# Kernel optimization log

Hardware: AMD Instinct MI355X
Metric: run time of the kernel (lower is better)

## Reference

```python
import jax, jax.numpy as jnp
import numpy as np

N_NODES = 50000
N_EDGES = 640000
IN_CH, HID_CH, OUT_CH = 128, 128, 64


def setup_inputs() -> dict:
    key = jax.random.key(0)
    ks = jax.random.split(key, 12)
    def glorot(k, fan_in, fan_out):
        s = jnp.sqrt(6.0 / (fan_in + fan_out))
        return jax.random.uniform(k, (fan_in, fan_out), jnp.float32, -s, s)
    x = jax.random.normal(ks[0], (N_NODES, IN_CH), jnp.float32)
    edge_index = jax.random.randint(ks[1], (2, N_EDGES), 0, N_NODES, jnp.int64)
    return {
        "x": x,
        "edge_index": edge_index,
        "W1": glorot(ks[2], IN_CH, HID_CH), "b1": jnp.zeros((HID_CH,), jnp.float32),
        "W2": glorot(ks[3], HID_CH, HID_CH), "b2": jnp.zeros((HID_CH,), jnp.float32),
        "W3": glorot(ks[4], HID_CH, OUT_CH), "b3": jnp.zeros((OUT_CH,), jnp.float32),
        "Wres": glorot(ks[5], IN_CH, OUT_CH), "bres": jnp.zeros((OUT_CH,), jnp.float32),
    }


def _gcn_norm(edge_index, n):
    # add self-loops, then symmetric normalization deg^-1/2[row]*deg^-1/2[col]
    sl = jnp.arange(n, dtype=edge_index.dtype)
    row = jnp.concatenate([edge_index[0], sl])
    col = jnp.concatenate([edge_index[1], sl])
    deg = jnp.zeros((n,), jnp.float32).at[col].add(1.0)
    dinv = jnp.where(deg > 0, jax.lax.rsqrt(deg), 0.0)
    norm = dinv[row] * dinv[col]  # [E+N]
    return row, col, norm


def _gcn_conv(x, W, b, row, col, norm, n):
    h = x @ W                          # linear transform first (PyG GCNConv)
    msg = h[row] * norm[:, None]       # gather + scale: [E+N, d]
    out = jax.ops.segment_sum(msg, col, num_segments=n)  # scatter-add
    return out + b


def reference(x, edge_index, W1, b1, W2, b2, W3, b3, Wres, bres):
    n = x.shape[0]
    row, col, norm = _gcn_norm(edge_index, n)
    # dropout is inference-mode identity (training=False)
    h = jax.nn.relu(_gcn_conv(x, W1, b1, row, col, norm, n))
    h = jax.nn.relu(_gcn_conv(h, W2, b2, row, col, norm, n))
    h = _gcn_conv(h, W3, b3, row, col, norm, n)
    residual = x @ Wres + bres
    return h + residual
```

## Files before the change

kernel.cpp:

```cpp
#include <hip/hip_runtime.h>

#define N_NODES 50000
#define N_EDGES 640000


__global__ void k_init(int* __restrict__ cnt, int* __restrict__ cursor) {
    int i = blockIdx.x * blockDim.x + threadIdx.x;
    if (i < N_NODES) { cnt[i] = 0; cursor[i] = 0; }
}

__global__ void k_count(const int* __restrict__ ei, int* __restrict__ cnt) {
    int e = blockIdx.x * blockDim.x + threadIdx.x;
    if (e < N_EDGES) atomicAdd(&cnt[ei[N_EDGES + e]], 1);
}

__global__ void k_dinv(const int* __restrict__ cnt, float* __restrict__ dinv) {
    int i = blockIdx.x * blockDim.x + threadIdx.x;
    if (i < N_NODES) dinv[i] = rsqrtf((float)(cnt[i] + 1));
}


__global__ void k_scan1(const int* __restrict__ cnt, int* __restrict__ offsets,
                        int* __restrict__ partials) {
    __shared__ int s[256];
    int t = threadIdx.x;
    int i = blockIdx.x * 256 + t;
    int v = (i < N_NODES) ? cnt[i] : 0;
    s[t] = v;
    __syncthreads();
    #pragma unroll
    for (int d = 1; d < 256; d <<= 1) {
        int add = (t >= d) ? s[t - d] : 0;
        __syncthreads();
        s[t] += add;
        __syncthreads();
    }
    if (i < N_NODES) offsets[i + 1] = s[t];
    if (t == 255) partials[blockIdx.x] = s[255];
    if (i == 0) offsets[0] = 0;
}

__global__ void k_scan2(int* __restrict__ partials, int nb) {
    __shared__ int s[256];
    int t = threadIdx.x;
    int v = (t < nb) ? partials[t] : 0;
    s[t] = v;
    __syncthreads();
    #pragma unroll
    for (int d = 1; d < 256; d <<= 1) {
        int add = (t >= d) ? s[t - d] : 0;
        __syncthreads();
        s[t] += add;
        __syncthreads();
    }
    if (t < nb) partials[t] = s[t] - v;
}

__global__ void k_scan3(int* __restrict__ offsets, const int* __restrict__ partials) {
    int i = blockIdx.x * 256 + threadIdx.x;
    if (i < N_NODES) offsets[i + 1] += partials[blockIdx.x];
}


__global__ void k_fill(const int* __restrict__ ei, const float* __restrict__ dinv,
                       const int* __restrict__ offsets, int* __restrict__ cursor,
                       int* __restrict__ csr_src, float* __restrict__ csr_w) {
    int e = blockIdx.x * blockDim.x + threadIdx.x;
    if (e < N_EDGES) {
        int r = ei[e];
        int c = ei[N_EDGES + e];
        float w = dinv[r] * dinv[c];
        int p = atomicAdd(&cursor[c], 1);
        int idx = offsets[c] + p;
        csr_src[idx] = r;
        csr_w[idx] = w;
    }
}


template <int OUTC>
__global__ __launch_bounds__(256, (OUTC == 128 ? 2 : 3))
void k_gemm(const float* __restrict__ A, const float* __restrict__ W,
            const float* __restrict__ bias, float* __restrict__ C) {
    constexpr int CG = OUTC / 4;
    constexpr int TR = CG / 8;
    __shared__ float sW[128 * OUTC];
    __shared__ float sX[32 * 128];

    int t = threadIdx.x;
    int row0 = blockIdx.x * 32;

    for (int i = t; i < 128 * OUTC / 4; i += 256)
        ((float4*)sW)[i] = ((const float4*)W)[i];
    for (int i = t; i < 1024; i += 256) {
        int r = i >> 5, c4 = i & 31;
        int gr = row0 + r;
        float4 v = make_float4(0.f, 0.f, 0.f, 0.f);
        if (gr < N_NODES) v = ((const float4*)(A + (size_t)gr * 128))[c4];
        ((float4*)sX)[i] = v;
    }
    __syncthreads();

    int tx = t % CG;
    int ty = t / CG;
    float acc[TR][4];
    #pragma unroll
    for (int rr = 0; rr < TR; ++rr) { acc[rr][0]=0.f; acc[rr][1]=0.f; acc[rr][2]=0.f; acc[rr][3]=0.f; }

    #pragma unroll 8
    for (int k = 0; k < 128; ++k) {
        float4 wv = ((const float4*)sW)[k * CG + tx];
        #pragma unroll
        for (int rr = 0; rr < TR; ++rr) {
            float xv = sX[(ty * TR + rr) * 128 + k];
            acc[rr][0] = fmaf(xv, wv.x, acc[rr][0]);
            acc[rr][1] = fmaf(xv, wv.y, acc[rr][1]);
            acc[rr][2] = fmaf(xv, wv.z, acc[rr][2]);
            acc[rr][3] = fmaf(xv, wv.w, acc[rr][3]);
        }
    }

    float4 bv = make_float4(0.f, 0.f, 0.f, 0.f);
    if (bias) bv = ((const float4*)bias)[tx];
    #pragma unroll
    for (int rr = 0; rr < TR; ++rr) {
        int gr = row0 + ty * TR + rr;
        if (gr < N_NODES) {
            float4 o = make_float4(acc[rr][0] + bv.x, acc[rr][1] + bv.y,
                                   acc[rr][2] + bv.z, acc[rr][3] + bv.w);
            ((float4*)(C + (size_t)gr * OUTC))[tx] = o;
        }
    }
}


template <int CH, bool RELU, bool HASADD>
__global__ __launch_bounds__(256)
void k_agg(const float* __restrict__ T, const int* __restrict__ offs,
           const int* __restrict__ csr_src, const float* __restrict__ csr_w,
           const float* __restrict__ dinv, const float* __restrict__ bias,
           const float* __restrict__ add, float* __restrict__ O) {
    int lane = threadIdx.x & 63;
    int v = blockIdx.x * 4 + (threadIdx.x >> 6);
    if (v >= N_NODES) return;
    int beg = offs[v], end = offs[v + 1];
    float di = dinv[v];
    float sw = di * di;

    if constexpr (CH == 128) {
        float2 hself = ((const float2*)(T + (size_t)v * 128))[lane];
        float a0 = sw * hself.x, a1 = sw * hself.y;
        int j = beg;
        for (; j + 4 <= end; j += 4) {
            int   s0 = csr_src[j],   s1 = csr_src[j+1], s2 = csr_src[j+2], s3 = csr_src[j+3];
            float w0 = csr_w[j],     w1 = csr_w[j+1],   w2 = csr_w[j+2],   w3 = csr_w[j+3];
            float2 h0 = ((const float2*)(T + (size_t)s0 * 128))[lane];
            float2 h1 = ((const float2*)(T + (size_t)s1 * 128))[lane];
            float2 h2 = ((const float2*)(T + (size_t)s2 * 128))[lane];
            float2 h3 = ((const float2*)(T + (size_t)s3 * 128))[lane];
            a0 = fmaf(w0, h0.x, fmaf(w1, h1.x, fmaf(w2, h2.x, fmaf(w3, h3.x, a0))));
            a1 = fmaf(w0, h0.y, fmaf(w1, h1.y, fmaf(w2, h2.y, fmaf(w3, h3.y, a1))));
        }
        for (; j < end; ++j) {
            int s = csr_src[j]; float w = csr_w[j];
            float2 hh = ((const float2*)(T + (size_t)s * 128))[lane];
            a0 = fmaf(w, hh.x, a0);
            a1 = fmaf(w, hh.y, a1);
        }
        a0 += bias[2 * lane];
        a1 += bias[2 * lane + 1];
        if constexpr (HASADD) {
            a0 += add[(size_t)v * 128 + 2 * lane];
            a1 += add[(size_t)v * 128 + 2 * lane + 1];
        }
        if constexpr (RELU) { a0 = fmaxf(a0, 0.f); a1 = fmaxf(a1, 0.f); }
        ((float2*)(O + (size_t)v * 128))[lane] = make_float2(a0, a1);
    } else {
        float a = sw * T[(size_t)v * 64 + lane];
        int j = beg;
        for (; j + 4 <= end; j += 4) {
            int   s0 = csr_src[j],   s1 = csr_src[j+1], s2 = csr_src[j+2], s3 = csr_src[j+3];
            float w0 = csr_w[j],     w1 = csr_w[j+1],   w2 = csr_w[j+2],   w3 = csr_w[j+3];
            float h0 = T[(size_t)s0 * 64 + lane];
            float h1 = T[(size_t)s1 * 64 + lane];
            float h2 = T[(size_t)s2 * 64 + lane];
            float h3 = T[(size_t)s3 * 64 + lane];
            a = fmaf(w0, h0, fmaf(w1, h1, fmaf(w2, h2, fmaf(w3, h3, a))));
        }
        for (; j < end; ++j) {
            int s = csr_src[j]; float w = csr_w[j];
            a = fmaf(w, T[(size_t)s * 64 + lane], a);
        }
        a += bias[lane];
        if constexpr (HASADD) a += add[(size_t)v * 64 + lane];
        if constexpr (RELU) a = fmaxf(a, 0.f);
        O[(size_t)v * 64 + lane] = a;
    }
}


extern "C" void kernel_launch(void* const* d_in, const int* in_sizes, int n_in,
                              void* d_out, int out_size, void* d_ws, size_t ws_size,
                              hipStream_t stream) {
    const float* x    = (const float*)d_in[0];
    const int*   ei   = (const int*)d_in[1];
    const float* W1   = (const float*)d_in[2];
    const float* b1   = (const float*)d_in[3];
    const float* W2   = (const float*)d_in[4];
    const float* b2   = (const float*)d_in[5];
    const float* W3   = (const float*)d_in[6];
    const float* b3   = (const float*)d_in[7];
    const float* Wres = (const float*)d_in[8];
    const float* bres = (const float*)d_in[9];
    float* out = (float*)d_out;

    char* base = (char*)d_ws;
    int*   cnt      = (int*)(base);
    int*   cursor   = (int*)(base + 200704);
    float* dinv     = (float*)(base + 2 * 200704);
    int*   offsets  = (int*)(base + 3 * 200704);
    int*   partials = (int*)(base + 4 * 200704);
    int*   csr_src  = (int*)(base + 4 * 200704 + 1024);
    float* csr_w    = (float*)(base + 4 * 200704 + 1024 + 2560000);
    float* bufA     = (float*)(base + 4 * 200704 + 1024 + 2 * 2560000);
    float* bufB     = bufA + (size_t)N_NODES * 128;

    const int NB_N = (N_NODES + 255) / 256;
    const int NB_E = (N_EDGES + 255) / 256;
    const int NB_G = (N_NODES + 31) / 32;
    const int NB_A = (N_NODES + 3) / 4;

    k_init <<<NB_N, 256, 0, stream>>>(cnt, cursor);
    k_count<<<NB_E, 256, 0, stream>>>(ei, cnt);
    k_dinv <<<NB_N, 256, 0, stream>>>(cnt, dinv);
    k_scan1<<<NB_N, 256, 0, stream>>>(cnt, offsets, partials);
    k_scan2<<<1,    256, 0, stream>>>(partials, NB_N);
    k_scan3<<<NB_N, 256, 0, stream>>>(offsets, partials);
    k_fill <<<NB_E, 256, 0, stream>>>(ei, dinv, offsets, cursor, csr_src, csr_w);

    k_gemm<128><<<NB_G, 256, 0, stream>>>(x, W1, nullptr, bufA);
    k_agg<128, true, false><<<NB_A, 256, 0, stream>>>(bufA, offsets, csr_src, csr_w, dinv, b1, nullptr, bufB);
    k_gemm<128><<<NB_G, 256, 0, stream>>>(bufB, W2, nullptr, bufA);
    k_agg<128, true, false><<<NB_A, 256, 0, stream>>>(bufA, offsets, csr_src, csr_w, dinv, b2, nullptr, bufB);
    k_gemm<64><<<NB_G, 256, 0, stream>>>(bufB, W3, nullptr, bufA);
    k_gemm<64><<<NB_G, 256, 0, stream>>>(x, Wres, bres, bufB);
    k_agg<64, false, true><<<NB_A, 256, 0, stream>>>(bufA, offsets, csr_src, csr_w, dinv, b3, bufB, out);
}
```

Before: 416.8 us.

## Fuse GCN aggregation with following GEMM and residual via shared-memory tiles

Each aggregation kernel now gathers 128 nodes into shared memory and immediately multiplies them by the next layer's weight matrix, so the intermediate aggregated activations never go to global memory. The final layer also computes the residual x@Wres+bres in the same kernel, and the dinv computation is folded into the scan. This removes several launches and global round trips. In exchange, weights are read straight from global/L1 instead of LDS, the 64KB LDS tile and 512-thread blocks limit occupancy, and each wave handles 16 nodes serially, which reduces the latency hiding available for the gather.

```diff
diff --git a/kernel.cpp b/kernel.cpp
--- a/kernel.cpp
+++ b/kernel.cpp
@@ -14,18 +14,13 @@
     if (e < N_EDGES) atomicAdd(&cnt[ei[N_EDGES + e]], 1);
 }
 
-__global__ void k_dinv(const int* __restrict__ cnt, float* __restrict__ dinv) {
-    int i = blockIdx.x * blockDim.x + threadIdx.x;
-    if (i < N_NODES) dinv[i] = rsqrtf((float)(cnt[i] + 1));
-}
-
-
 __global__ void k_scan1(const int* __restrict__ cnt, int* __restrict__ offsets,
-                        int* __restrict__ partials) {
+                        int* __restrict__ partials, float* __restrict__ dinv) {
     __shared__ int s[256];
     int t = threadIdx.x;
     int i = blockIdx.x * 256 + t;
     int v = (i < N_NODES) ? cnt[i] : 0;
+    if (i < N_NODES) dinv[i] = rsqrtf((float)(v + 1));
     s[t] = v;
     __syncthreads();
     #pragma unroll
@@ -60,7 +55,6 @@
     int i = blockIdx.x * 256 + threadIdx.x;
     if (i < N_NODES) offsets[i + 1] += partials[blockIdx.x];
 }
-
 
 __global__ void k_fill(const int* __restrict__ ei, const float* __restrict__ dinv,
                        const int* __restrict__ offsets, int* __restrict__ cursor,
@@ -78,123 +72,209 @@
 }
 
 
+__global__ __launch_bounds__(512, 4)
+void k_gemm_x(const float* __restrict__ A, const float* __restrict__ W,
+              float* __restrict__ O) {
+    int t = threadIdx.x;
+    int tx = t & 31;
+    int ty = t >> 5;
+    int base = blockIdx.x * 128;
+
+    float acc[8][4];
+    #pragma unroll
+    for (int r = 0; r < 8; ++r) { acc[r][0]=0.f; acc[r][1]=0.f; acc[r][2]=0.f; acc[r][3]=0.f; }
+
+    int rows[8];
+    #pragma unroll
+    for (int r = 0; r < 8; ++r) {
+        int gr = base + ty * 8 + r;
+        rows[r] = (gr < N_NODES) ? gr : (N_NODES - 1);
+    }
+
+    #pragma unroll 2
+    for (int k = 0; k < 128; k += 4) {
+        float4 w0 = ((const float4*)(W + (size_t)(k + 0) * 128))[tx];
+        float4 w1 = ((const float4*)(W + (size_t)(k + 1) * 128))[tx];
+        float4 w2 = ((const float4*)(W + (size_t)(k + 2) * 128))[tx];
+        float4 w3 = ((const float4*)(W + (size_t)(k + 3) * 128))[tx];
+        #pragma unroll
+        for (int r = 0; r < 8; ++r) {
+            float4 xv = *(const float4*)(A + (size_t)rows[r] * 128 + k);
+            acc[r][0] = fmaf(xv.x, w0.x, fmaf(xv.y, w1.x, fmaf(xv.z, w2.x, fmaf(xv.w, w3.x, acc[r][0]))));
+            acc[r][1] = fmaf(xv.x, w0.y, fmaf(xv.y, w1.y, fmaf(xv.z, w2.y, fmaf(xv.w, w3.y, acc[r][1]))));
+            acc[r][2] = fmaf(xv.x, w0.z, fmaf(xv.y, w1.z, fmaf(xv.z, w2.z, fmaf(xv.w, w3.z, acc[r][2]))));
+            acc[r][3] = fmaf(xv.x, w0.w, fmaf(xv.y, w1.w, fmaf(xv.z, w2.w, fmaf(xv.w, w3.w, acc[r][3]))));
+        }
+    }
+
+    #pragma unroll
+    for (int r = 0; r < 8; ++r) {
+        int gr = base + ty * 8 + r;
+        if (gr < N_NODES)
+            ((float4*)(O + (size_t)gr * 128))[tx] =
+                make_float4(acc[r][0], acc[r][1], acc[r][2], acc[r][3]);
+    }
+}
+
+
 template <int OUTC>
-__global__ __launch_bounds__(256, (OUTC == 128 ? 2 : 3))
-void k_gemm(const float* __restrict__ A, const float* __restrict__ W,
-            const float* __restrict__ bias, float* __restrict__ C) {
+__global__ __launch_bounds__(512, 4)
+void k_agg_gemm(const float* __restrict__ T, const int* __restrict__ offs,
+                const int* __restrict__ csr_src, const float* __restrict__ csr_w,
+                const float* __restrict__ dinv, const float* __restrict__ ba,
+                const float* __restrict__ W, float* __restrict__ O) {
+    __shared__ float sh[128 * 128];
+    int t = threadIdx.x;
+    int wave = t >> 6, lane = t & 63;
+    int base = blockIdx.x * 128;
+
+    for (int i = 0; i < 16; ++i) {
+        int vl = wave * 16 + i;
+        int v = base + vl;
+        float a0 = 0.f, a1 = 0.f;
+        if (v < N_NODES) {
+            float di = dinv[v];
+            float sw = di * di;
+            float2 hs = ((const float2*)(T + (size_t)v * 128))[lane];
+            a0 = sw * hs.x; a1 = sw * hs.y;
+            int beg = offs[v], end = offs[v + 1];
+            int j = beg;
+            for (; j + 4 <= end; j += 4) {
+                int   s0 = csr_src[j],   s1 = csr_src[j+1], s2 = csr_src[j+2], s3 = csr_src[j+3];
+                float w0 = csr_w[j],     w1 = csr_w[j+1],   w2 = csr_w[j+2],   w3 = csr_w[j+3];
+                float2 h0 = ((const float2*)(T + (size_t)s0 * 128))[lane];
+                float2 h1 = ((const float2*)(T + (size_t)s1 * 128))[lane];
+                float2 h2 = ((const float2*)(T + (size_t)s2 * 128))[lane];
+                float2 h3 = ((const float2*)(T + (size_t)s3 * 128))[lane];
+                a0 = fmaf(w0, h0.x, fmaf(w1, h1.x, fmaf(w2, h2.x, fmaf(w3, h3.x, a0))));
+                a1 = fmaf(w0, h0.y, fmaf(w1, h1.y, fmaf(w2, h2.y, fmaf(w3, h3.y, a1))));
+            }
+            for (; j < end; ++j) {
+                int s = csr_src[j]; float w = csr_w[j];
+                float2 hh = ((const float2*)(T + (size_t)s * 128))[lane];
+                a0 = fmaf(w, hh.x, a0);
+                a1 = fmaf(w, hh.y, a1);
+            }
+            a0 = fmaxf(a0 + ba[2 * lane], 0.f);
+            a1 = fmaxf(a1 + ba[2 * lane + 1], 0.f);
+        }
+        ((float2*)(sh + vl * 128))[lane] = make_float2(a0, a1);
+    }
+    __syncthreads();
+
     constexpr int CG = OUTC / 4;
-    constexpr int TR = CG / 8;
-    __shared__ float sW[128 * OUTC];
-    __shared__ float sX[32 * 128];
-
-    int t = threadIdx.x;
-    int row0 = blockIdx.x * 32;
-
-    for (int i = t; i < 128 * OUTC / 4; i += 256)
-        ((float4*)sW)[i] = ((const float4*)W)[i];
-    for (int i = t; i < 1024; i += 256) {
-        int r = i >> 5, c4 = i & 31;
-        int gr = row0 + r;
-        float4 v = make_float4(0.f, 0.f, 0.f, 0.f);
-        if (gr < N_NODES) v = ((const float4*)(A + (size_t)gr * 128))[c4];
-        ((float4*)sX)[i] = v;
-    }
-    __syncthreads();
-
+    constexpr int TR = CG / 4;
     int tx = t % CG;
     int ty = t / CG;
+
     float acc[TR][4];
     #pragma unroll
-    for (int rr = 0; rr < TR; ++rr) { acc[rr][0]=0.f; acc[rr][1]=0.f; acc[rr][2]=0.f; acc[rr][3]=0.f; }
-
-    #pragma unroll 8
-    for (int k = 0; k < 128; ++k) {
-        float4 wv = ((const float4*)sW)[k * CG + tx];
+    for (int r = 0; r < TR; ++r) { acc[r][0]=0.f; acc[r][1]=0.f; acc[r][2]=0.f; acc[r][3]=0.f; }
+
+    #pragma unroll 2
+    for (int k = 0; k < 128; k += 4) {
+        float4 w0 = ((const float4*)(W + (size_t)(k + 0) * OUTC))[tx];
+        float4 w1 = ((const float4*)(W + (size_t)(k + 1) * OUTC))[tx];
+        float4 w2 = ((const float4*)(W + (size_t)(k + 2) * OUTC))[tx];
+        float4 w3 = ((const float4*)(W + (size_t)(k + 3) * OUTC))[tx];
         #pragma unroll
-        for (int rr = 0; rr < TR; ++rr) {
-            float xv = sX[(ty * TR + rr) * 128 + k];
-            acc[rr][0] = fmaf(xv, wv.x, acc[rr][0]);
-            acc[rr][1] = fmaf(xv, wv.y, acc[rr][1]);
-            acc[rr][2] = fmaf(xv, wv.z, acc[rr][2]);
-            acc[rr][3] = fmaf(xv, wv.w, acc[rr][3]);
-        }
-    }
-
-    float4 bv = make_float4(0.f, 0.f, 0.f, 0.f);
-    if (bias) bv = ((const float4*)bias)[tx];
-    #pragma unroll
-    for (int rr = 0; rr < TR; ++rr) {
-        int gr = row0 + ty * TR + rr;
+        for (int r = 0; r < TR; ++r) {
+            float4 xv = *(const float4*)(sh + (ty * TR + r) * 128 + k);
+            acc[r][0] = fmaf(xv.x, w0.x, fmaf(xv.y, w1.x, fmaf(xv.z, w2.x, fmaf(xv.w, w3.x, acc[r][0]))));
+            acc[r][1] = fmaf(xv.x, w0.y, fmaf(xv.y, w1.y, fmaf(xv.z, w2.y, fmaf(xv.w, w3.y, acc[r][1]))));
+            acc[r][2] = fmaf(xv.x, w0.z, fmaf(xv.y, w1.z, fmaf(xv.z, w2.z, fmaf(xv.w, w3.z, acc[r][2]))));
+            acc[r][3] = fmaf(xv.x, w0.w, fmaf(xv.y, w1.w, fmaf(xv.z, w2.w, fmaf(xv.w, w3.w, acc[r][3]))));
+        }
+    }
+
+    #pragma unroll
+    for (int r = 0; r < TR; ++r) {
+        int gr = base + ty * TR + r;
+        if (gr < N_NODES)
+            ((float4*)(O + (size_t)gr * OUTC))[tx] =
+                make_float4(acc[r][0], acc[r][1], acc[r][2], acc[r][3]);
+    }
+}
+
+
+__global__ __launch_bounds__(512, 4)
+void k_agg64_res(const float* __restrict__ T, const int* __restrict__ offs,
+                 const int* __restrict__ csr_src, const float* __restrict__ csr_w,
+                 const float* __restrict__ dinv, const float* __restrict__ b3,
+                 const float* __restrict__ x, const float* __restrict__ Wres,
+                 const float* __restrict__ bres, float* __restrict__ out) {
+    __shared__ float sh[128 * 64];
+    int t = threadIdx.x;
+    int wave = t >> 6, lane = t & 63;
+    int base = blockIdx.x * 128;
+
+    for (int i = 0; i < 16; ++i) {
+        int vl = wave * 16 + i;
+        int v = base + vl;
+        float a = 0.f;
+        if (v < N_NODES) {
+            float di = dinv[v];
+            float sw = di * di;
+            a = sw * T[(size_t)v * 64 + lane];
+            int beg = offs[v], end = offs[v + 1];
+            int j = beg;
+            for (; j + 4 <= end; j += 4) {
+                int   s0 = csr_src[j],   s1 = csr_src[j+1], s2 = csr_src[j+2], s3 = csr_src[j+3];
+                float w0 = csr_w[j],     w1 = csr_w[j+1],   w2 = csr_w[j+2],   w3 = csr_w[j+3];
+                float h0 = T[(size_t)s0 * 64 + lane];
+                float h1 = T[(size_t)s1 * 64 + lane];
+                float h2 = T[(size_t)s2 * 64 + lane];
+                float h3 = T[(size_t)s3 * 64 + lane];
+                a = fmaf(w0, h0, fmaf(w1, h1, fmaf(w2, h2, fmaf(w3, h3, a))));
+            }
+            for (; j < end; ++j)
+                a = fmaf(csr_w[j], T[(size_t)csr_src[j] * 64 + lane], a);
+            a += b3[lane];
+        }
+        sh[vl * 64 + lane] = a;
+    }
+    __syncthreads();
+
+    int tx = t & 15;
+    int ty = t >> 4;
+    float acc[4][4];
+    #pragma unroll
+    for (int r = 0; r < 4; ++r) { acc[r][0]=0.f; acc[r][1]=0.f; acc[r][2]=0.f; acc[r][3]=0.f; }
+
+    int rows[4];
+    #pragma unroll
+    for (int r = 0; r < 4; ++r) {
+        int gr = base + ty * 4 + r;
+        rows[r] = (gr < N_NODES) ? gr : (N_NODES - 1);
+    }
+
+    #pragma unroll 2
+    for (int k = 0; k < 128; k += 4) {
+        float4 w0 = ((const float4*)(Wres + (size_t)(k + 0) * 64))[tx];
+        float4 w1 = ((const float4*)(Wres + (size_t)(k + 1) * 64))[tx];
+        float4 w2 = ((const float4*)(Wres + (size_t)(k + 2) * 64))[tx];
+        float4 w3 = ((const float4*)(Wres + (size_t)(k + 3) * 64))[tx];
+        #pragma unroll
+        for (int r = 0; r < 4; ++r) {
+            float4 xv = *(const float4*)(x + (size_t)rows[r] * 128 + k);
+            acc[r][0] = fmaf(xv.x, w0.x, fmaf(xv.y, w1.x, fmaf(xv.z, w2.x, fmaf(xv.w, w3.x, acc[r][0]))));
+            acc[r][1] = fmaf(xv.x, w0.y, fmaf(xv.y, w1.y, fmaf(xv.z, w2.y, fmaf(xv.w, w3.y, acc[r][1]))));
+            acc[r][2] = fmaf(xv.x, w0.z, fmaf(xv.y, w1.z, fmaf(xv.z, w2.z, fmaf(xv.w, w3.z, acc[r][2]))));
+            acc[r][3] = fmaf(xv.x, w0.w, fmaf(xv.y, w1.w, fmaf(xv.z, w2.w, fmaf(xv.w, w3.w, acc[r][3]))));
+        }
+    }
+
+    float4 bv = ((const float4*)bres)[tx];
+    #pragma unroll
+    for (int r = 0; r < 4; ++r) {
+        int vl = ty * 4 + r;
+        int gr = base + vl;
         if (gr < N_NODES) {
-            float4 o = make_float4(acc[rr][0] + bv.x, acc[rr][1] + bv.y,
-                                   acc[rr][2] + bv.z, acc[rr][3] + bv.w);
-            ((float4*)(C + (size_t)gr * OUTC))[tx] = o;
-        }
-    }
-}
-
-
-template <int CH, bool RELU, bool HASADD>
-__global__ __launch_bounds__(256)
-void k_agg(const float* __restrict__ T, const int* __restrict__ offs,
-           const int* __restrict__ csr_src, const float* __restrict__ csr_w,
-           const float* __restrict__ dinv, const float* __restrict__ bias,
-           const float* __restrict__ add, float* __restrict__ O) {
-    int lane = threadIdx.x & 63;
-    int v = blockIdx.x * 4 + (threadIdx.x >> 6);
-    if (v >= N_NODES) return;
-    int beg = offs[v], end = offs[v + 1];
-    float di = dinv[v];
-    float sw = di * di;
-
-    if constexpr (CH == 128) {
-        float2 hself = ((const float2*)(T + (size_t)v * 128))[lane];
-        float a0 = sw * hself.x, a1 = sw * hself.y;
-        int j = beg;
-        for (; j + 4 <= end; j += 4) {
-            int   s0 = csr_src[j],   s1 = csr_src[j+1], s2 = csr_src[j+2], s3 = csr_src[j+3];
-            float w0 = csr_w[j],     w1 = csr_w[j+1],   w2 = csr_w[j+2],   w3 = csr_w[j+3];
-            float2 h0 = ((const float2*)(T + (size_t)s0 * 128))[lane];
-            float2 h1 = ((const float2*)(T + (size_t)s1 * 128))[lane];
-            float2 h2 = ((const float2*)(T + (size_t)s2 * 128))[lane];
-            float2 h3 = ((const float2*)(T + (size_t)s3 * 128))[lane];
-            a0 = fmaf(w0, h0.x, fmaf(w1, h1.x, fmaf(w2, h2.x, fmaf(w3, h3.x, a0))));
-            a1 = fmaf(w0, h0.y, fmaf(w1, h1.y, fmaf(w2, h2.y, fmaf(w3, h3.y, a1))));
-        }
-        for (; j < end; ++j) {
-            int s = csr_src[j]; float w = csr_w[j];
-            float2 hh = ((const float2*)(T + (size_t)s * 128))[lane];
-            a0 = fmaf(w, hh.x, a0);
-            a1 = fmaf(w, hh.y, a1);
-        }
-        a0 += bias[2 * lane];
-        a1 += bias[2 * lane + 1];
-        if constexpr (HASADD) {
-            a0 += add[(size_t)v * 128 + 2 * lane];
-            a1 += add[(size_t)v * 128 + 2 * lane + 1];
-        }
-        if constexpr (RELU) { a0 = fmaxf(a0, 0.f); a1 = fmaxf(a1, 0.f); }
-        ((float2*)(O + (size_t)v * 128))[lane] = make_float2(a0, a1);
-    } else {
-        float a = sw * T[(size_t)v * 64 + lane];
-        int j = beg;
-        for (; j + 4 <= end; j += 4) {
-            int   s0 = csr_src[j],   s1 = csr_src[j+1], s2 = csr_src[j+2], s3 = csr_src[j+3];
-            float w0 = csr_w[j],     w1 = csr_w[j+1],   w2 = csr_w[j+2],   w3 = csr_w[j+3];
-            float h0 = T[(size_t)s0 * 64 + lane];
-            float h1 = T[(size_t)s1 * 64 + lane];
-            float h2 = T[(size_t)s2 * 64 + lane];
-            float h3 = T[(size_t)s3 * 64 + lane];
-            a = fmaf(w0, h0, fmaf(w1, h1, fmaf(w2, h2, fmaf(w3, h3, a))));
-        }
-        for (; j < end; ++j) {
-            int s = csr_src[j]; float w = csr_w[j];
-            a = fmaf(w, T[(size_t)s * 64 + lane], a);
-        }
-        a += bias[lane];
-        if constexpr (HASADD) a += add[(size_t)v * 64 + lane];
-        if constexpr (RELU) a = fmaxf(a, 0.f);
-        O[(size_t)v * 64 + lane] = a;
+            float4 s = ((const float4*)(sh + vl * 64))[tx];
+            ((float4*)(out + (size_t)gr * 64))[tx] =
+                make_float4(acc[r][0] + bv.x + s.x, acc[r][1] + bv.y + s.y,
+                            acc[r][2] + bv.z + s.z, acc[r][3] + bv.w + s.w);
+        }
     }
 }
 
@@ -227,22 +307,17 @@
 
     const int NB_N = (N_NODES + 255) / 256;
     const int NB_E = (N_EDGES + 255) / 256;
-    const int NB_G = (N_NODES + 31) / 32;
-    const int NB_A = (N_NODES + 3) / 4;
+    const int NB_F = (N_NODES + 127) / 128;
 
     k_init <<<NB_N, 256, 0, stream>>>(cnt, cursor);
     k_count<<<NB_E, 256, 0, stream>>>(ei, cnt);
-    k_dinv <<<NB_N, 256, 0, stream>>>(cnt, dinv);
-    k_scan1<<<NB_N, 256, 0, stream>>>(cnt, offsets, partials);
+    k_scan1<<<NB_N, 256, 0, stream>>>(cnt, offsets, partials, dinv);
     k_scan2<<<1,    256, 0, stream>>>(partials, NB_N);
     k_scan3<<<NB_N, 256, 0, stream>>>(offsets, partials);
     k_fill <<<NB_E, 256, 0, stream>>>(ei, dinv, offsets, cursor, csr_src, csr_w);
 
-    k_gemm<128><<<NB_G, 256, 0, stream>>>(x, W1, nullptr, bufA);
-    k_agg<128, true, false><<<NB_A, 256, 0, stream>>>(bufA, offsets, csr_src, csr_w, dinv, b1, nullptr, bufB);
-    k_gemm<128><<<NB_G, 256, 0, stream>>>(bufB, W2, nullptr, bufA);
-    k_agg<128, true, false><<<NB_A, 256, 0, stream>>>(bufA, offsets, csr_src, csr_w, dinv, b2, nullptr, bufB);
-    k_gemm<64><<<NB_G, 256, 0, stream>>>(bufB, W3, nullptr, bufA);
-    k_gemm<64><<<NB_G, 256, 0, stream>>>(x, Wres, bres, bufB);
-    k_agg<64, false, true><<<NB_A, 256, 0, stream>>>(bufA, offsets, csr_src, csr_w, dinv, b3, bufB, out);
-}
+    k_gemm_x<<<NB_F, 512, 0, stream>>>(x, W1, bufA);
+    k_agg_gemm<128><<<NB_F, 512, 0, stream>>>(bufA, offsets, csr_src, csr_w, dinv, b1, W2, bufB);
+    k_agg_gemm<64><<<NB_F, 512, 0, stream>>>(bufB, offsets, csr_src, csr_w, dinv, b2, W3, bufA);
+    k_agg64_res<<<NB_F, 512, 0, stream>>>(bufA, offsets, csr_src, csr_w, dinv, b3, x, Wres, bres, out);
+}
```

Measured after the change: 494.9 us. 1.19x slower.

## Store transformed features in fp16 for gathers and drop shared-memory GEMM tiling

Applied to the files above, without the earlier changes.

The GEMM outputs that feed each aggregation are now written as fp16, so the irregular neighbour gathers move half the bytes. The GEMM drops its shared-memory staging of W and X. Each thread instead reads W and A directly from global memory/cache over an 8-row register tile, and the occupancy hint is raised. The degree-inverse computation is folded into the first scan kernel to remove one launch. The fp16 intermediates lose precision relative to the fp32 reference, and the GEMM now relies on cache hits instead of LDS reuse.

```diff
diff --git a/kernel.cpp b/kernel.cpp
--- a/kernel.cpp
+++ b/kernel.cpp
@@ -1,4 +1,5 @@
 #include <hip/hip_runtime.h>
+#include <hip/hip_fp16.h>
 
 #define N_NODES 50000
 #define N_EDGES 640000
@@ -14,18 +15,13 @@
     if (e < N_EDGES) atomicAdd(&cnt[ei[N_EDGES + e]], 1);
 }
 
-__global__ void k_dinv(const int* __restrict__ cnt, float* __restrict__ dinv) {
-    int i = blockIdx.x * blockDim.x + threadIdx.x;
-    if (i < N_NODES) dinv[i] = rsqrtf((float)(cnt[i] + 1));
-}
-
-
 __global__ void k_scan1(const int* __restrict__ cnt, int* __restrict__ offsets,
-                        int* __restrict__ partials) {
+                        int* __restrict__ partials, float* __restrict__ dinv) {
     __shared__ int s[256];
     int t = threadIdx.x;
     int i = blockIdx.x * 256 + t;
     int v = (i < N_NODES) ? cnt[i] : 0;
+    if (i < N_NODES) dinv[i] = rsqrtf((float)(v + 1));
     s[t] = v;
     __syncthreads();
     #pragma unroll
@@ -60,7 +56,6 @@
     int i = blockIdx.x * 256 + threadIdx.x;
     if (i < N_NODES) offsets[i + 1] += partials[blockIdx.x];
 }
-
 
 __global__ void k_fill(const int* __restrict__ ei, const float* __restrict__ dinv,
                        const int* __restrict__ offsets, int* __restrict__ cursor,
@@ -78,65 +73,75 @@
 }
 
 
-template <int OUTC>
-__global__ __launch_bounds__(256, (OUTC == 128 ? 2 : 3))
+template <int OUTC, bool HALF_OUT>
+__global__ __launch_bounds__(256, 4)
 void k_gemm(const float* __restrict__ A, const float* __restrict__ W,
-            const float* __restrict__ bias, float* __restrict__ C) {
+            const float* __restrict__ bias, void* __restrict__ O) {
     constexpr int CG = OUTC / 4;
-    constexpr int TR = CG / 8;
-    __shared__ float sW[128 * OUTC];
-    __shared__ float sX[32 * 128];
+    constexpr int RG = 256 / CG;
+    constexpr int TR = 8;
+    constexpr int BM = RG * TR;
 
     int t = threadIdx.x;
-    int row0 = blockIdx.x * 32;
-
-    for (int i = t; i < 128 * OUTC / 4; i += 256)
-        ((float4*)sW)[i] = ((const float4*)W)[i];
-    for (int i = t; i < 1024; i += 256) {
-        int r = i >> 5, c4 = i & 31;
-        int gr = row0 + r;
-        float4 v = make_float4(0.f, 0.f, 0.f, 0.f);
-        if (gr < N_NODES) v = ((const float4*)(A + (size_t)gr * 128))[c4];
-        ((float4*)sX)[i] = v;
-    }
-    __syncthreads();
-
     int tx = t % CG;
     int ty = t / CG;
+    int base = blockIdx.x * BM;
+
     float acc[TR][4];
     #pragma unroll
-    for (int rr = 0; rr < TR; ++rr) { acc[rr][0]=0.f; acc[rr][1]=0.f; acc[rr][2]=0.f; acc[rr][3]=0.f; }
-
-    #pragma unroll 8
-    for (int k = 0; k < 128; ++k) {
-        float4 wv = ((const float4*)sW)[k * CG + tx];
+    for (int r = 0; r < TR; ++r) { acc[r][0]=0.f; acc[r][1]=0.f; acc[r][2]=0.f; acc[r][3]=0.f; }
+
+    int rows[TR];
+    #pragma unroll
+    for (int r = 0; r < TR; ++r) {
+        int gr = base + ty * TR + r;
+        rows[r] = (gr < N_NODES) ? gr : (N_NODES - 1);
+    }
+
+    #pragma unroll 2
+    for (int k = 0; k < 128; k += 4) {
+        float4 w0 = ((const float4*)(W + (size_t)(k + 0) * OUTC))[tx];
+        float4 w1 = ((const float4*)(W + (size_t)(k + 1) * OUTC))[tx];
+        float4 w2 = ((const float4*)(W + (size_t)(k + 2) * OUTC))[tx];
+        float4 w3 = ((const float4*)(W + (size_t)(k + 3) * OUTC))[tx];
         #pragma unroll
-        for (int rr = 0; rr < TR; ++rr) {
-            float xv = sX[(ty * TR + rr) * 128 + k];
-            acc[rr][0] = fmaf(xv, wv.x, acc[rr][0]);
-            acc[rr][1] = fmaf(xv, wv.y, acc[rr][1]);
-            acc[rr][2] = fmaf(xv, wv.z, acc[rr][2]);
-            acc[rr][3] = fmaf(xv, wv.w, acc[rr][3]);
+        for (int r = 0; r < TR; ++r) {
+            float4 xv = *(const float4*)(A + (size_t)rows[r] * 128 + k);
+            acc[r][0] = fmaf(xv.x, w0.x, fmaf(xv.y, w1.x, fmaf(xv.z, w2.x, fmaf(xv.w, w3.x, acc[r][0]))));
+            acc[r][1] = fmaf(xv.x, w0.y, fmaf(xv.y, w1.y, fmaf(xv.z, w2.y, fmaf(xv.w, w3.y, acc[r][1]))));
+            acc[r][2] = fmaf(xv.x, w0.z, fmaf(xv.y, w1.z, fmaf(xv.z, w2.z, fmaf(xv.w, w3.z, acc[r][2]))));
+            acc[r][3] = fmaf(xv.x, w0.w, fmaf(xv.y, w1.w, fmaf(xv.z, w2.w, fmaf(xv.w, w3.w, acc[r][3]))));
         }
     }
 
     float4 bv = make_float4(0.f, 0.f, 0.f, 0.f);
     if (bias) bv = ((const float4*)bias)[tx];
     #pragma unroll
-    for (int rr = 0; rr < TR; ++rr) {
-        int gr = row0 + ty * TR + rr;
+    for (int r = 0; r < TR; ++r) {
+        int gr = base + ty * TR + r;
         if (gr < N_NODES) {
-            float4 o = make_float4(acc[rr][0] + bv.x, acc[rr][1] + bv.y,
-                                   acc[rr][2] + bv.z, acc[rr][3] + bv.w);
-            ((float4*)(C + (size_t)gr * OUTC))[tx] = o;
-        }
-    }
-}
-
-
-template <int CH, bool RELU, bool HASADD>
+            if constexpr (HALF_OUT) {
+                __half* Oh = (__half*)O;
+                ushort4 p = make_ushort4(
+                    __half_as_ushort(__float2half_rn(acc[r][0] + bv.x)),
+                    __half_as_ushort(__float2half_rn(acc[r][1] + bv.y)),
+                    __half_as_ushort(__float2half_rn(acc[r][2] + bv.z)),
+                    __half_as_ushort(__float2half_rn(acc[r][3] + bv.w)));
+                *(ushort4*)(Oh + (size_t)gr * OUTC + tx * 4) = p;
+            } else {
+                float* Of = (float*)O;
+                ((float4*)(Of + (size_t)gr * OUTC))[tx] =
+                    make_float4(acc[r][0] + bv.x, acc[r][1] + bv.y,
+                                acc[r][2] + bv.z, acc[r][3] + bv.w);
+            }
+        }
+    }
+}
+
+
+template <int CH, bool RELU, bool HASADD, bool HALF_IN>
 __global__ __launch_bounds__(256)
-void k_agg(const float* __restrict__ T, const int* __restrict__ offs,
+void k_agg(const void* __restrict__ Tv, const int* __restrict__ offs,
            const int* __restrict__ csr_src, const float* __restrict__ csr_w,
            const float* __restrict__ dinv, const float* __restrict__ bias,
            const float* __restrict__ add, float* __restrict__ O) {
@@ -148,22 +153,28 @@
     float sw = di * di;
 
     if constexpr (CH == 128) {
-        float2 hself = ((const float2*)(T + (size_t)v * 128))[lane];
-        float a0 = sw * hself.x, a1 = sw * hself.y;
+        auto LD = [&](int s) -> float2 {
+            if constexpr (HALF_IN)
+                return __half22float2(((const __half2*)((const __half*)Tv + (size_t)s * 128))[lane]);
+            else
+                return ((const float2*)((const float*)Tv + (size_t)s * 128))[lane];
+        };
+        float2 hs = LD(v);
+        float a0 = sw * hs.x, a1 = sw * hs.y;
         int j = beg;
         for (; j + 4 <= end; j += 4) {
             int   s0 = csr_src[j],   s1 = csr_src[j+1], s2 = csr_src[j+2], s3 = csr_src[j+3];
             float w0 = csr_w[j],     w1 = csr_w[j+1],   w2 = csr_w[j+2],   w3 = csr_w[j+3];
-            float2 h0 = ((const float2*)(T + (size_t)s0 * 128))[lane];
-            float2 h1 = ((const float2*)(T + (size_t)s1 * 128))[lane];
-            float2 h2 = ((const float2*)(T + (size_t)s2 * 128))[lane];
-            float2 h3 = ((const float2*)(T + (size_t)s3 * 128))[lane];
+            float2 h0 = LD(s0);
+            float2 h1 = LD(s1);
+            float2 h2 = LD(s2);
+            float2 h3 = LD(s3);
             a0 = fmaf(w0, h0.x, fmaf(w1, h1.x, fmaf(w2, h2.x, fmaf(w3, h3.x, a0))));
             a1 = fmaf(w0, h0.y, fmaf(w1, h1.y, fmaf(w2, h2.y, fmaf(w3, h3.y, a1))));
         }
         for (; j < end; ++j) {
-            int s = csr_src[j]; float w = csr_w[j];
-            float2 hh = ((const float2*)(T + (size_t)s * 128))[lane];
+            float w = csr_w[j];
+            float2 hh = LD(csr_src[j]);
             a0 = fmaf(w, hh.x, a0);
             a1 = fmaf(w, hh.y, a1);
         }
@@ -176,21 +187,25 @@
         if constexpr (RELU) { a0 = fmaxf(a0, 0.f); a1 = fmaxf(a1, 0.f); }
         ((float2*)(O + (size_t)v * 128))[lane] = make_float2(a0, a1);
     } else {
-        float a = sw * T[(size_t)v * 64 + lane];
+        auto LD1 = [&](int s) -> float {
+            if constexpr (HALF_IN)
+                return __half2float(((const __half*)Tv)[(size_t)s * 64 + lane]);
+            else
+                return ((const float*)Tv)[(size_t)s * 64 + lane];
+        };
+        float a = sw * LD1(v);
         int j = beg;
         for (; j + 4 <= end; j += 4) {
             int   s0 = csr_src[j],   s1 = csr_src[j+1], s2 = csr_src[j+2], s3 = csr_src[j+3];
             float w0 = csr_w[j],     w1 = csr_w[j+1],   w2 = csr_w[j+2],   w3 = csr_w[j+3];
-            float h0 = T[(size_t)s0 * 64 + lane];
-            float h1 = T[(size_t)s1 * 64 + lane];
-            float h2 = T[(size_t)s2 * 64 + lane];
-            float h3 = T[(size_t)s3 * 64 + lane];
+            float h0 = LD1(s0);
+            float h1 = LD1(s1);
+            float h2 = LD1(s2);
+            float h3 = LD1(s3);
             a = fmaf(w0, h0, fmaf(w1, h1, fmaf(w2, h2, fmaf(w3, h3, a))));
         }
-        for (; j < end; ++j) {
-            int s = csr_src[j]; float w = csr_w[j];
-            a = fmaf(w, T[(size_t)s * 64 + lane], a);
-        }
+        for (; j < end; ++j)
+            a = fmaf(csr_w[j], LD1(csr_src[j]), a);
         a += bias[lane];
         if constexpr (HASADD) a += add[(size_t)v * 64 + lane];
         if constexpr (RELU) a = fmaxf(a, 0.f);
@@ -215,34 +230,35 @@
     float* out = (float*)d_out;
 
     char* base = (char*)d_ws;
-    int*   cnt      = (int*)(base);
-    int*   cursor   = (int*)(base + 200704);
-    float* dinv     = (float*)(base + 2 * 200704);
-    int*   offsets  = (int*)(base + 3 * 200704);
-    int*   partials = (int*)(base + 4 * 200704);
-    int*   csr_src  = (int*)(base + 4 * 200704 + 1024);
-    float* csr_w    = (float*)(base + 4 * 200704 + 1024 + 2560000);
-    float* bufA     = (float*)(base + 4 * 200704 + 1024 + 2 * 2560000);
-    float* bufB     = bufA + (size_t)N_NODES * 128;
+    int*    cnt      = (int*)(base);
+    int*    cursor   = (int*)(base + 200704);
+    float*  dinv     = (float*)(base + 2 * 200704);
+    int*    offsets  = (int*)(base + 3 * 200704);
+    int*    partials = (int*)(base + 4 * 200704);
+    int*    csr_src  = (int*)(base + 4 * 200704 + 1024);
+    float*  csr_w    = (float*)(base + 4 * 200704 + 1024 + 2560000);
+    float*  bufA     = (float*)(base + 4 * 200704 + 1024 + 2 * 2560000);
+    float*  bufB     = bufA + (size_t)N_NODES * 128;
+    __half* bufH     = (__half*)(bufB + (size_t)N_NODES * 64);
 
     const int NB_N = (N_NODES + 255) / 256;
     const int NB_E = (N_EDGES + 255) / 256;
-    const int NB_G = (N_NODES + 31) / 32;
+    const int NB_G128 = (N_NODES + 63) / 64;
+    const int NB_G64  = (N_NODES + 127) / 128;
     const int NB_A = (N_NODES + 3) / 4;
 
     k_init <<<NB_N, 256, 0, stream>>>(cnt, cursor);
     k_count<<<NB_E, 256, 0, stream>>>(ei, cnt);
-    k_dinv <<<NB_N, 256, 0, stream>>>(cnt, dinv);
-    k_scan1<<<NB_N, 256, 0, stream>>>(cnt, offsets, partials);
+    k_scan1<<<NB_N, 256, 0, stream>>>(cnt, offsets, partials, dinv);
     k_scan2<<<1,    256, 0, stream>>>(partials, NB_N);
     k_scan3<<<NB_N, 256, 0, stream>>>(offsets, partials);
     k_fill <<<NB_E, 256, 0, stream>>>(ei, dinv, offsets, cursor, csr_src, csr_w);
 
-    k_gemm<128><<<NB_G, 256, 0, stream>>>(x, W1, nullptr, bufA);
-    k_agg<128, true, false><<<NB_A, 256, 0, stream>>>(bufA, offsets, csr_src, csr_w, dinv, b1, nullptr, bufB);
-    k_gemm<128><<<NB_G, 256, 0, stream>>>(bufB, W2, nullptr, bufA);
-    k_agg<128, true, false><<<NB_A, 256, 0, stream>>>(bufA, offsets, csr_src, csr_w, dinv, b2, nullptr, bufB);
-    k_gemm<64><<<NB_G, 256, 0, stream>>>(bufB, W3, nullptr, bufA);
-    k_gemm<64><<<NB_G, 256, 0, stream>>>(x, Wres, bres, bufB);
-    k_agg<64, false, true><<<NB_A, 256, 0, stream>>>(bufA, offsets, csr_src, csr_w, dinv, b3, bufB, out);
-}
+    k_gemm<128, true><<<NB_G128, 256, 0, stream>>>(x, W1, nullptr, (void*)bufH);
+    k_agg<128, true, false, true><<<NB_A, 256, 0, stream>>>((const void*)bufH, offsets, csr_src, csr_w, dinv, b1, nullptr, bufA);
+    k_gemm<128, true><<<NB_G128, 256, 0, stream>>>(bufA, W2, nullptr, (void*)bufH);
+    k_agg<128, true, false, true><<<NB_A, 256, 0, stream>>>((const void*)bufH, offsets, csr_src, csr_w, dinv, b2, nullptr, bufA);
+    k_gemm<64, true><<<NB_G64, 256, 0, stream>>>(bufA, W3, nullptr, (void*)bufH);
+    k_gemm<64, false><<<NB_G64, 256, 0, stream>>>(x, Wres, bres, (void*)bufB);
+    k_agg<64, false, true, true><<<NB_A, 256, 0, stream>>>((const void*)bufH, offsets, csr_src, csr_w, dinv, b3, bufB, out);
+}
```

After: 489.0 us. 1.17x slower.
